# Optimization experiments

Hardware: AMD Instinct MI355X
Metric: run time of the kernel (lower is better)

The kernel has to match this reference:

```python
import jax, jax.numpy as jnp
import numpy as np

B, S, D = 2, 2048, 1024
E, N, HID = 8, 4, 4096

def setup_inputs() -> dict:
    key = jax.random.key(0)
    ks = jax.random.split(key, 6)
    x = jax.random.normal(ks[0], (B, S, D), dtype=jnp.float32)
    w_router = jax.random.normal(ks[1], (E, D), dtype=jnp.float32) * 0.02
    A_fc = jax.random.normal(ks[2], (E, N, N, N), dtype=jnp.float32) * 0.5
    S_fc = jax.random.normal(ks[3], (E, N, HID // N, D // N), dtype=jnp.float32) * (1.0 / np.sqrt(D))
    A_proj = jax.random.normal(ks[4], (E, N, N, N), dtype=jnp.float32) * 0.5
    S_proj = jax.random.normal(ks[5], (E, N, D // N, HID // N), dtype=jnp.float32) * (1.0 / np.sqrt(HID))
    return {"x": x, "w_router": w_router, "A_fc": A_fc, "S_fc": S_fc, "A_proj": A_proj, "S_proj": S_proj}

def _phm(Xn, A, S):
    # Xn: [T, n, s_in], S: [n, s_out, s_in], A: [n, n, n] -> [T, n, s_out]
    T_ = jnp.einsum('bkl,iol->bkio', Xn, S)
    return jnp.einsum('ijk,bkio->bjo', A, T_)

def reference(x, w_router, A_fc, S_fc, A_proj, S_proj):
    e_num, n = A_fc.shape[0], A_fc.shape[1]
    d = x.shape[-1]
    flat = x.reshape(-1, d)                      # [T, D]
    T = flat.shape[0]
    logits = flat @ w_router.T                   # [T, E]
    probs = jax.nn.softmax(logits, axis=-1)
    expert_idx = jnp.argmax(logits, axis=-1)     # [T]
    tpe = jnp.zeros((e_num,), flat.dtype).at[expert_idx].add(1.0)
    frac = tpe / T
    aux_loss = jnp.sum(frac * probs.mean(axis=0)) * e_num
    Xn = flat.reshape(T, n, d // n)
    out = jnp.zeros_like(flat)
    for e in range(e_num):                        # small fixed expert loop
        h = _phm(Xn, A_fc[e], S_fc[e]).reshape(T, -1)   # [T, HID]
        h = jnp.where(h >= 0, h, 0.5 * h)               # leaky_relu slope 0.5
        Hn = (h * h).reshape(T, n, -1)
        y = _phm(Hn, A_proj[e], S_proj[e]).reshape(T, d)
        out = out + jnp.where((expert_idx == e)[:, None], y, jnp.zeros((), flat.dtype))
    return out.reshape(x.shape), aux_loss
```

## Files before the change

### kernel.cpp

```cpp
#include <hip/hip_runtime.h>
#include <hip/hip_bf16.h>


#define T_TOK 4096
#define DIM   1024
#define NEXP  8
#define HIDD  4096
#define SLOTS 5120

static constexpr size_t OFF_WFC   = 0;
static constexpr size_t OFF_WPROJ = 67108864ull;
static constexpr size_t OFF_XB    = 134217728ull;
static constexpr size_t OFF_H     = 144703488ull;
static constexpr size_t OFF_PROBS = 186646528ull;
static constexpr size_t OFF_EIDX  = OFF_PROBS + (size_t)T_TOK*8*4;
static constexpr size_t OFF_TOK   = OFF_EIDX + (size_t)T_TOK*4;
static constexpr size_t OFF_CNT   = OFF_TOK + (size_t)SLOTS*4;

typedef __attribute__((ext_vector_type(8))) short short8;
typedef __attribute__((ext_vector_type(4))) float f32x4;

static __device__ __forceinline__ ushort f2bf(float f) {
    __hip_bfloat16 h = __float2bfloat16(f);
    return __builtin_bit_cast(ushort, h);
}

static __device__ __forceinline__ void gload_lds16(const ushort* g, ushort* l) {
    __builtin_amdgcn_global_load_lds((const __attribute__((address_space(1))) void*)g,
                                     (__attribute__((address_space(3))) void*)l,
                                     16, 0, 0);
}

__global__ __launch_bounds__(256) void router_k(const float* __restrict__ x,
                                                const float* __restrict__ wr,
                                                float* __restrict__ probs,
                                                int* __restrict__ eidx,
                                                ushort* __restrict__ xb)
{
    int tid = threadIdx.x, w = tid >> 6, lane = tid & 63;
    int t = blockIdx.x * 4 + w;
    const float4* xr = (const float4*)(x + (size_t)t * DIM);
    float4 xv[4];
#pragma unroll
    for (int q = 0; q < 4; q++) xv[q] = xr[q * 64 + lane];
    ushort4* xo = (ushort4*)(xb + (size_t)t * DIM);
#pragma unroll
    for (int q = 0; q < 4; q++) {
        float4 v = xv[q];
        ushort4 bq;
        bq.x = f2bf(v.x); bq.y = f2bf(v.y); bq.z = f2bf(v.z); bq.w = f2bf(v.w);
        xo[q * 64 + lane] = bq;
    }
    double lg[8];
#pragma unroll
    for (int e = 0; e < 8; e++) {
        const float4* wv = (const float4*)(wr + (size_t)e * DIM);
        double s = 0.0;
#pragma unroll
        for (int q = 0; q < 4; q++) {
            float4 a = xv[q], b = wv[q * 64 + lane];
            s += (double)a.x * b.x + (double)a.y * b.y + (double)a.z * b.z + (double)a.w * b.w;
        }
#pragma unroll
        for (int d = 1; d < 64; d <<= 1) s += __shfl_xor(s, d);
        lg[e] = s;
    }
    double m = lg[0];
#pragma unroll
    for (int e = 1; e < 8; e++) m = lg[e] > m ? lg[e] : m;
    double ex[8], sum = 0.0;
#pragma unroll
    for (int e = 0; e < 8; e++) { ex[e] = exp(lg[e] - m); sum += ex[e]; }
    if (lane < 8) probs[(size_t)t * 8 + lane] = (float)(ex[lane] / sum);
    if (lane == 0) {
        int am = 0; double bv = lg[0];
#pragma unroll
        for (int e = 1; e < 8; e++) if (lg[e] > bv) { bv = lg[e]; am = e; }
        eidx[t] = am;
    }
}

__global__ __launch_bounds__(256) void plan_k(const float* __restrict__ probs,
                                              const int* __restrict__ eidx,
                                              int* __restrict__ counts,
                                              int* __restrict__ offsets,
                                              int* __restrict__ tok,
                                              float* __restrict__ auxout)
{
    __shared__ int hist[256][8];
    __shared__ double red[256][8];
    __shared__ int offs[8];
    int tid = threadIdx.x;
    for (int i = tid; i < SLOTS; i += 256) tok[i] = -1;
    int base = tid * 16;
    int le[16];
    int lc[8] = {0,0,0,0,0,0,0,0};
#pragma unroll
    for (int j = 0; j < 16; j++) { le[j] = eidx[base + j]; lc[le[j]]++; }
#pragma unroll
    for (int e = 0; e < 8; e++) hist[tid][e] = lc[e];
    __syncthreads();
    for (int s = 1; s < 256; s <<= 1) {
        int v[8];
        if (tid >= s) {
#pragma unroll
            for (int e = 0; e < 8; e++) v[e] = hist[tid - s][e];
        }
        __syncthreads();
        if (tid >= s) {
#pragma unroll
            for (int e = 0; e < 8; e++) hist[tid][e] += v[e];
        }
        __syncthreads();
    }
    int myBase[8];
#pragma unroll
    for (int e = 0; e < 8; e++) myBase[e] = hist[tid][e] - lc[e];
    if (tid == 0) {
        int off = 0;
#pragma unroll
        for (int e = 0; e < 8; e++) {
            int c = hist[255][e];
            counts[e] = c;
            offsets[e] = off; offs[e] = off;
            off += (c + 127) & ~127;
        }
    }
    __syncthreads();
    int cur[8];
#pragma unroll
    for (int e = 0; e < 8; e++) cur[e] = myBase[e];
#pragma unroll
    for (int j = 0; j < 16; j++) {
        int e = le[j];
        tok[offs[e] + cur[e]++] = base + j;
    }
    double ps[8] = {0, 0, 0, 0, 0, 0, 0, 0};
    for (int t = tid; t < T_TOK; t += 256) {
#pragma unroll
        for (int e = 0; e < 8; e++) ps[e] += (double)probs[(size_t)t * 8 + e];
    }
#pragma unroll
    for (int e = 0; e < 8; e++) red[tid][e] = ps[e];
    __syncthreads();
    for (int s = 128; s > 0; s >>= 1) {
        if (tid < s) {
#pragma unroll
            for (int e = 0; e < 8; e++) red[tid][e] += red[tid + s][e];
        }
        __syncthreads();
    }
    if (tid == 0) {
        double aux = 0.0;
#pragma unroll
        for (int e = 0; e < 8; e++)
            aux += ((double)hist[255][e] / T_TOK) * (red[0][e] / T_TOK);
        auxout[0] = (float)(aux * NEXP);
    }
}

__global__ __launch_bounds__(256) void wfc_k(const float* __restrict__ A,
                                             const float* __restrict__ S,
                                             ushort* __restrict__ W)
{
    int b = blockIdx.x;
    int e = b >> 10, o = b & 1023;
    int l = threadIdx.x;
    __shared__ float Ash[64];
    if (l < 64) Ash[l] = A[e * 64 + l];
    __syncthreads();
    float s0 = S[((size_t)(e * 4 + 0) * 1024 + o) * 256 + l];
    float s1 = S[((size_t)(e * 4 + 1) * 1024 + o) * 256 + l];
    float s2 = S[((size_t)(e * 4 + 2) * 1024 + o) * 256 + l];
    float s3 = S[((size_t)(e * 4 + 3) * 1024 + o) * 256 + l];
    size_t base = (size_t)e * 4194304ull;
#pragma unroll
    for (int j = 0; j < 4; j++)
#pragma unroll
        for (int k = 0; k < 4; k++) {
            float v = Ash[j * 4 + k] * s0 + Ash[16 + j * 4 + k] * s1 +
                      Ash[32 + j * 4 + k] * s2 + Ash[48 + j * 4 + k] * s3;
            W[base + (size_t)(j * 1024 + o) * 1024 + k * 256 + l] = f2bf(v);
        }
}

__global__ __launch_bounds__(256) void wpj_k(const float* __restrict__ A,
                                             const float* __restrict__ S,
                                             ushort* __restrict__ W)
{
    int b = blockIdx.x;
    int e = b >> 8, o = b & 255;
    int tid = threadIdx.x;
    __shared__ float Ash[64];
    if (tid < 64) Ash[tid] = A[e * 64 + tid];
    __syncthreads();
    float s[4][4];
#pragma unroll
    for (int i = 0; i < 4; i++)
#pragma unroll
        for (int q = 0; q < 4; q++)
            s[i][q] = S[((size_t)(e * 4 + i) * 256 + o) * 1024 + q * 256 + tid];
    size_t base = (size_t)e * 4194304ull;
#pragma unroll
    for (int j = 0; j < 4; j++)
#pragma unroll
        for (int k = 0; k < 4; k++) {
            float a0 = Ash[j * 4 + k], a1 = Ash[16 + j * 4 + k];
            float a2 = Ash[32 + j * 4 + k], a3 = Ash[48 + j * 4 + k];
#pragma unroll
            for (int q = 0; q < 4; q++) {
                float v = a0 * s[0][q] + a1 * s[1][q] + a2 * s[2][q] + a3 * s[3][q];
                W[base + (size_t)(j * 256 + o) * 4096 + k * 1024 + q * 256 + tid] = f2bf(v);
            }
        }
}

template <int KDIM, int NDIM, int NSPLIT, bool FC>
__global__ __launch_bounds__(256, 2) void moe_gemm_k(const ushort* __restrict__ Abuf,
                                                     const ushort* __restrict__ Wbuf,
                                                     ushort* __restrict__ Hout,
                                                     float* __restrict__ Yout,
                                                     const int* __restrict__ counts,
                                                     const int* __restrict__ offsets,
                                                     const int* __restrict__ tok)
{
    __shared__ __align__(16) ushort As[128 * 64];
    __shared__ __align__(16) ushort Bs[256 * 64];
    constexpr int KSUB = KDIM / NSPLIT;
    constexpr int NT = KSUB / 64;
    int b = blockIdx.x;
    int nb, split, ms;
    if (FC) {
        int r = b >> 3;
        nb = (b & 7) * 2 + r / 40;
        split = 0;
        ms = r % 40;
    } else {
        nb = (b & 7) >> 1;
        split = b & 1;
        ms = b >> 3;
    }
    int e = -1, mt = 0, acct = 0;
#pragma unroll
    for (int i = 0; i < 8; i++) {
        int tiles = (counts[i] + 127) >> 7;
        if (e < 0 && ms < acct + tiles) { e = i; mt = ms - acct; }
        acct += tiles;
    }
    if (e < 0) return;
    int m_base = offsets[e] + mt * 128;
    int n_base = nb * 256;
    int tid = threadIdx.x, w = tid >> 6, lane = tid & 63;
    int wm = w >> 1, wn = w & 1;
    const ushort* Bb = Wbuf + (size_t)e * NDIM * KDIM + (size_t)n_base * KDIM;
    int lr = lane >> 3;
    int lcs = (((lane & 7) ^ lr) << 3);
    const ushort* arow[4];
#pragma unroll
    for (int i = 0; i < 4; i++) {
        int sl = m_base + i * 32 + w * 8 + lr;
        int rt = sl;
        if (FC) { rt = tok[sl]; if (rt < 0) rt = 0; }
        arow[i] = Abuf + (size_t)rt * KDIM + lcs;
    }
    f32x4 acc[4][8];
#pragma unroll
    for (int i = 0; i < 4; i++)
#pragma unroll
        for (int j = 0; j < 8; j++) acc[i][j] = (f32x4){0.f, 0.f, 0.f, 0.f};

    for (int t = 0; t < NT; t++) {
        int k0 = split * KSUB + t * 64;
#pragma unroll
        for (int i = 0; i < 4; i++)
            gload_lds16(arow[i] + k0, &As[(i * 32 + w * 8) * 64]);
#pragma unroll
        for (int i = 0; i < 8; i++) {
            int r0 = i * 32 + w * 8;
            gload_lds16(Bb + (size_t)(r0 + lr) * KDIM + k0 + lcs, &Bs[r0 * 64]);
        }
        __syncthreads();
#pragma unroll
        for (int ks = 0; ks < 2; ks++) {
            short8 a[4], bfr[8];
#pragma unroll
            for (int f = 0; f < 4; f++) {
                int ra = wm * 64 + f * 16 + (lane & 15);
                int ca = (((ks * 4 + (lane >> 4)) ^ (lane & 7)) << 3);
                a[f] = *(const short8*)&As[ra * 64 + ca];
            }
#pragma unroll
            for (int f = 0; f < 8; f++) {
                int rb = wn * 128 + f * 16 + (lane & 15);
                int ca = (((ks * 4 + (lane >> 4)) ^ (lane & 7)) << 3);
                bfr[f] = *(const short8*)&Bs[rb * 64 + ca];
            }
#pragma unroll
            for (int mf = 0; mf < 4; mf++)
#pragma unroll
                for (int nf = 0; nf < 8; nf++)
                    acc[mf][nf] = __builtin_amdgcn_mfma_f32_16x16x32_bf16(a[mf], bfr[nf], acc[mf][nf], 0, 0, 0);
        }
        __syncthreads();
    }

    int col0 = n_base + wn * 128;
    int row0 = wm * 64 + (lane >> 4) * 4;
    if (FC) {
#pragma unroll
        for (int mf = 0; mf < 4; mf++)
#pragma unroll
            for (int nf = 0; nf < 8; nf++) {
                int col = col0 + nf * 16 + (lane & 15);
#pragma unroll
                for (int rg = 0; rg < 4; rg++) {
                    float v = acc[mf][nf][rg];
                    v = v >= 0.f ? v : 0.5f * v;
                    v = v * v;
                    Hout[(size_t)(m_base + row0 + mf * 16 + rg) * NDIM + col] = f2bf(v);
                }
            }
    } else {
        float* P = Yout + (size_t)split * SLOTS * NDIM;
#pragma unroll
        for (int mf = 0; mf < 4; mf++)
#pragma unroll
            for (int nf = 0; nf < 8; nf++) {
                int col = col0 + nf * 16 + (lane & 15);
#pragma unroll
                for (int rg = 0; rg < 4; rg++)
                    P[(size_t)(m_base + row0 + mf * 16 + rg) * NDIM + col] = acc[mf][nf][rg];
            }
    }
}

__global__ __launch_bounds__(256) void reduce_k(const float* __restrict__ P,
                                                const int* __restrict__ tok,
                                                float* __restrict__ out)
{
    int slot = blockIdx.x;
    int t = tok[slot];
    if (t < 0) return;
    const float4* p0 = (const float4*)(P + (size_t)slot * DIM);
    const float4* p1 = (const float4*)(P + (size_t)(SLOTS + slot) * DIM);
    float4* o = (float4*)(out + (size_t)t * DIM);
    int i = threadIdx.x;
    float4 a = p0[i], b = p1[i];
    o[i] = (float4){a.x + b.x, a.y + b.y, a.z + b.z, a.w + b.w};
}

extern "C" void kernel_launch(void* const* d_in, const int* in_sizes, int n_in,
                              void* d_out, int out_size, void* d_ws, size_t ws_size,
                              hipStream_t stream)
{
    const float* x    = (const float*)d_in[0];
    const float* wr   = (const float*)d_in[1];
    const float* A_fc = (const float*)d_in[2];
    const float* S_fc = (const float*)d_in[3];
    const float* A_pj = (const float*)d_in[4];
    const float* S_pj = (const float*)d_in[5];
    float* out = (float*)d_out;
    char* ws = (char*)d_ws;

    ushort* Wfc   = (ushort*)(ws + OFF_WFC);
    float*  Part  = (float*)(ws + OFF_WFC);
    ushort* Wpj   = (ushort*)(ws + OFF_WPROJ);
    ushort* xb    = (ushort*)(ws + OFF_XB);
    ushort* h     = (ushort*)(ws + OFF_H);
    float*  probs = (float*)(ws + OFF_PROBS);
    int*    eidx  = (int*)(ws + OFF_EIDX);
    int*    tok   = (int*)(ws + OFF_TOK);
    int*    counts  = (int*)(ws + OFF_CNT);
    int*    offsets = counts + 16;

    router_k<<<T_TOK / 4, 256, 0, stream>>>(x, wr, probs, eidx, xb);
    plan_k<<<1, 256, 0, stream>>>(probs, eidx, counts, offsets, tok,
                                  out + (size_t)T_TOK * DIM);
    wfc_k<<<NEXP * 1024, 256, 0, stream>>>(A_fc, S_fc, Wfc);
    wpj_k<<<NEXP * 256, 256, 0, stream>>>(A_pj, S_pj, Wpj);
    moe_gemm_k<1024, 4096, 1, true><<<640, 256, 0, stream>>>(xb, Wfc, h, nullptr, counts, offsets, tok);
    moe_gemm_k<4096, 1024, 2, false><<<320, 256, 0, stream>>>(h, Wpj, nullptr, Part, counts, offsets, tok);
    reduce_k<<<SLOTS, 256, 0, stream>>>(Part, tok, out);
}
```

Baseline: 190.9 us.

## Triple-buffer MoE GEMM LDS tiles with 512-thread blocks and async prefetch

Restructures the expert GEMM kernel to use 8 waves per block (2x4 wave grid, 64x64 per wave) and a three-stage LDS ring buffer. The next-next K tile is prefetched with direct-to-LDS loads while the current one is computed, using explicit vmcnt waits and raw barriers in place of two __syncthreads per iteration. MFMA sections are wrapped in s_setprio. The aim is to hide global-load latency and raise occupancy, at the cost of triple the LDS footprint (144KB per block), which may limit resident blocks per CU.

Result: slower. 229.6 us (+20.3%).

```diff
diff --git a/kernel.cpp b/kernel.cpp
--- a/kernel.cpp
+++ b/kernel.cpp
@@ -216,7 +216,7 @@
 }
 
 template <int KDIM, int NDIM, int NSPLIT, bool FC>
-__global__ __launch_bounds__(256, 2) void moe_gemm_k(const ushort* __restrict__ Abuf,
+__global__ __launch_bounds__(512, 4) void moe_gemm_k(const ushort* __restrict__ Abuf,
                                                      const ushort* __restrict__ Wbuf,
                                                      ushort* __restrict__ Hout,
                                                      float* __restrict__ Yout,
@@ -224,8 +224,8 @@
                                                      const int* __restrict__ offsets,
                                                      const int* __restrict__ tok)
 {
-    __shared__ __align__(16) ushort As[128 * 64];
-    __shared__ __align__(16) ushort Bs[256 * 64];
+    __shared__ __align__(16) ushort As[3][128 * 64];
+    __shared__ __align__(16) ushort Bs[3][256 * 64];
     constexpr int KSUB = KDIM / NSPLIT;
     constexpr int NT = KSUB / 64;
     int b = blockIdx.x;
@@ -251,66 +251,78 @@
     int m_base = offsets[e] + mt * 128;
     int n_base = nb * 256;
     int tid = threadIdx.x, w = tid >> 6, lane = tid & 63;
-    int wm = w >> 1, wn = w & 1;
+    int wm = w >> 2, wn = w & 3;
     const ushort* Bb = Wbuf + (size_t)e * NDIM * KDIM + (size_t)n_base * KDIM;
     int lr = lane >> 3;
     int lcs = (((lane & 7) ^ lr) << 3);
-    const ushort* arow[4];
-#pragma unroll
-    for (int i = 0; i < 4; i++) {
-        int sl = m_base + i * 32 + w * 8 + lr;
+    int kbase = split * KSUB;
+    const ushort* arow[2];
+#pragma unroll
+    for (int i = 0; i < 2; i++) {
+        int sl = m_base + i * 64 + w * 8 + lr;
         int rt = sl;
         if (FC) { rt = tok[sl]; if (rt < 0) rt = 0; }
-        arow[i] = Abuf + (size_t)rt * KDIM + lcs;
-    }
-    f32x4 acc[4][8];
+        arow[i] = Abuf + (size_t)rt * KDIM + kbase + lcs;
+    }
+    const ushort* brow[4];
 #pragma unroll
     for (int i = 0; i < 4; i++)
-#pragma unroll
-        for (int j = 0; j < 8; j++) acc[i][j] = (f32x4){0.f, 0.f, 0.f, 0.f};
-
+        brow[i] = Bb + (size_t)(i * 64 + w * 8 + lr) * KDIM + kbase + lcs;
+
+    f32x4 acc[4][4];
+#pragma unroll
+    for (int i = 0; i < 4; i++)
+#pragma unroll
+        for (int j = 0; j < 4; j++) acc[i][j] = (f32x4){0.f, 0.f, 0.f, 0.f};
+
+    auto STAGE = [&](int kt, int q) {
+        int k0 = kt * 64;
+#pragma unroll
+        for (int i = 0; i < 2; i++)
+            gload_lds16(arow[i] + k0, &As[q][(i * 64 + w * 8) * 64]);
+#pragma unroll
+        for (int i = 0; i < 4; i++)
+            gload_lds16(brow[i] + k0, &Bs[q][(i * 64 + w * 8) * 64]);
+    };
+
+    STAGE(0, 0);
+    STAGE(1, 1);
+
+    int q = 0;
     for (int t = 0; t < NT; t++) {
-        int k0 = split * KSUB + t * 64;
-#pragma unroll
-        for (int i = 0; i < 4; i++)
-            gload_lds16(arow[i] + k0, &As[(i * 32 + w * 8) * 64]);
-#pragma unroll
-        for (int i = 0; i < 8; i++) {
-            int r0 = i * 32 + w * 8;
-            gload_lds16(Bb + (size_t)(r0 + lr) * KDIM + k0 + lcs, &Bs[r0 * 64]);
-        }
-        __syncthreads();
+        if (t == NT - 1) { asm volatile("s_waitcnt vmcnt(0)" ::: "memory"); }
+        else             { asm volatile("s_waitcnt vmcnt(6)" ::: "memory"); }
+        __builtin_amdgcn_s_barrier();
+        __builtin_amdgcn_sched_barrier(0);
+        if (t + 2 < NT) STAGE(t + 2, (q + 2) % 3);
 #pragma unroll
         for (int ks = 0; ks < 2; ks++) {
-            short8 a[4], bfr[8];
+            short8 a[4], bb[4];
+            int ca = (((ks * 4 + (lane >> 4)) ^ (lane & 7)) << 3);
 #pragma unroll
             for (int f = 0; f < 4; f++) {
-                int ra = wm * 64 + f * 16 + (lane & 15);
-                int ca = (((ks * 4 + (lane >> 4)) ^ (lane & 7)) << 3);
-                a[f] = *(const short8*)&As[ra * 64 + ca];
+                a[f]  = *(const short8*)&As[q][(wm * 64 + f * 16 + (lane & 15)) * 64 + ca];
+                bb[f] = *(const short8*)&Bs[q][(wn * 64 + f * 16 + (lane & 15)) * 64 + ca];
             }
-#pragma unroll
-            for (int f = 0; f < 8; f++) {
-                int rb = wn * 128 + f * 16 + (lane & 15);
-                int ca = (((ks * 4 + (lane >> 4)) ^ (lane & 7)) << 3);
-                bfr[f] = *(const short8*)&Bs[rb * 64 + ca];
-            }
+            __builtin_amdgcn_s_setprio(1);
 #pragma unroll
             for (int mf = 0; mf < 4; mf++)
 #pragma unroll
-                for (int nf = 0; nf < 8; nf++)
-                    acc[mf][nf] = __builtin_amdgcn_mfma_f32_16x16x32_bf16(a[mf], bfr[nf], acc[mf][nf], 0, 0, 0);
-        }
-        __syncthreads();
-    }
-
-    int col0 = n_base + wn * 128;
+                for (int nf = 0; nf < 4; nf++)
+                    acc[mf][nf] = __builtin_amdgcn_mfma_f32_16x16x32_bf16(a[mf], bb[nf], acc[mf][nf], 0, 0, 0);
+            __builtin_amdgcn_s_setprio(0);
+        }
+        __builtin_amdgcn_s_barrier();
+        q = (q + 1) % 3;
+    }
+
+    int col0 = n_base + wn * 64;
     int row0 = wm * 64 + (lane >> 4) * 4;
     if (FC) {
 #pragma unroll
         for (int mf = 0; mf < 4; mf++)
 #pragma unroll
-            for (int nf = 0; nf < 8; nf++) {
+            for (int nf = 0; nf < 4; nf++) {
                 int col = col0 + nf * 16 + (lane & 15);
 #pragma unroll
                 for (int rg = 0; rg < 4; rg++) {
@@ -325,7 +337,7 @@
 #pragma unroll
         for (int mf = 0; mf < 4; mf++)
 #pragma unroll
-            for (int nf = 0; nf < 8; nf++) {
+            for (int nf = 0; nf < 4; nf++) {
                 int col = col0 + nf * 16 + (lane & 15);
 #pragma unroll
                 for (int rg = 0; rg < 4; rg++)
@@ -378,7 +390,7 @@
                                   out + (size_t)T_TOK * DIM);
     wfc_k<<<NEXP * 1024, 256, 0, stream>>>(A_fc, S_fc, Wfc);
     wpj_k<<<NEXP * 256, 256, 0, stream>>>(A_pj, S_pj, Wpj);
-    moe_gemm_k<1024, 4096, 1, true><<<640, 256, 0, stream>>>(xb, Wfc, h, nullptr, counts, offsets, tok);
-    moe_gemm_k<4096, 1024, 2, false><<<320, 256, 0, stream>>>(h, Wpj, nullptr, Part, counts, offsets, tok);
+    moe_gemm_k<1024, 4096, 1, true><<<640, 512, 0, stream>>>(xb, Wfc, h, nullptr, counts, offsets, tok);
+    moe_gemm_k<4096, 1024, 2, false><<<320, 512, 0, stream>>>(h, Wpj, nullptr, Part, counts, offsets, tok);
     reduce_k<<<SLOTS, 256, 0, stream>>>(Part, tok, out);
 }
```

## Drop split-K and reduce pass, scatter proj output directly; merge weight kernels

Applied to the files above, without the earlier changes.

The projection GEMM no longer splits K in two with a separate reduce kernel. It now uses 64-row M tiles with four N-slices per block and scatters results straight to the output rows via the token map. The two weight-construction kernels are merged into one launch. The router emits per-block prob sums instead of per-token probs, so the planner reads less. This removes the partial-buffer write/read and two launches, at the cost of longer per-block K loops and a different tile shape for the proj GEMM.

Result: slower. 195.3 us (+2.3%).

```diff
diff --git a/kernel.cpp b/kernel.cpp
--- a/kernel.cpp
+++ b/kernel.cpp
@@ -12,8 +12,8 @@
 static constexpr size_t OFF_WPROJ = 67108864ull;
 static constexpr size_t OFF_XB    = 134217728ull;
 static constexpr size_t OFF_H     = 144703488ull;
-static constexpr size_t OFF_PROBS = 186646528ull;
-static constexpr size_t OFF_EIDX  = OFF_PROBS + (size_t)T_TOK*8*4;
+static constexpr size_t OFF_BSUM  = 186646528ull;
+static constexpr size_t OFF_EIDX  = OFF_BSUM + 1024*8*8;
 static constexpr size_t OFF_TOK   = OFF_EIDX + (size_t)T_TOK*4;
 static constexpr size_t OFF_CNT   = OFF_TOK + (size_t)SLOTS*4;
 
@@ -33,10 +33,11 @@
 
 __global__ __launch_bounds__(256) void router_k(const float* __restrict__ x,
                                                 const float* __restrict__ wr,
-                                                float* __restrict__ probs,
+                                                double* __restrict__ bsum,
                                                 int* __restrict__ eidx,
                                                 ushort* __restrict__ xb)
 {
+    __shared__ double shp[4][8];
     int tid = threadIdx.x, w = tid >> 6, lane = tid & 63;
     int t = blockIdx.x * 4 + w;
     const float4* xr = (const float4*)(x + (size_t)t * DIM);
@@ -71,16 +72,20 @@
     double ex[8], sum = 0.0;
 #pragma unroll
     for (int e = 0; e < 8; e++) { ex[e] = exp(lg[e] - m); sum += ex[e]; }
-    if (lane < 8) probs[(size_t)t * 8 + lane] = (float)(ex[lane] / sum);
+    if (lane < 8) shp[w][lane] = ex[lane] / sum;
     if (lane == 0) {
         int am = 0; double bv = lg[0];
 #pragma unroll
         for (int e = 1; e < 8; e++) if (lg[e] > bv) { bv = lg[e]; am = e; }
         eidx[t] = am;
     }
-}
-
-__global__ __launch_bounds__(256) void plan_k(const float* __restrict__ probs,
+    __syncthreads();
+    if (tid < 8)
+        bsum[(size_t)blockIdx.x * 8 + tid] =
+            shp[0][tid] + shp[1][tid] + shp[2][tid] + shp[3][tid];
+}
+
+__global__ __launch_bounds__(256) void plan_k(const double* __restrict__ bsum,
                                               const int* __restrict__ eidx,
                                               int* __restrict__ counts,
                                               int* __restrict__ offsets,
@@ -136,9 +141,9 @@
         tok[offs[e] + cur[e]++] = base + j;
     }
     double ps[8] = {0, 0, 0, 0, 0, 0, 0, 0};
-    for (int t = tid; t < T_TOK; t += 256) {
-#pragma unroll
-        for (int e = 0; e < 8; e++) ps[e] += (double)probs[(size_t)t * 8 + e];
+    for (int b = tid; b < 1024; b += 256) {
+#pragma unroll
+        for (int e = 0; e < 8; e++) ps[e] += bsum[(size_t)b * 8 + e];
     }
 #pragma unroll
     for (int e = 0; e < 8; e++) red[tid][e] = ps[e];
@@ -159,63 +164,61 @@
     }
 }
 
-__global__ __launch_bounds__(256) void wfc_k(const float* __restrict__ A,
-                                             const float* __restrict__ S,
-                                             ushort* __restrict__ W)
-{
+__global__ __launch_bounds__(256) void wmat_k(const float* __restrict__ Afc,
+                                              const float* __restrict__ Sfc,
+                                              const float* __restrict__ Apj,
+                                              const float* __restrict__ Spj,
+                                              ushort* __restrict__ Wfc,
+                                              ushort* __restrict__ Wpj)
+{
+    __shared__ float Ash[64];
     int b = blockIdx.x;
-    int e = b >> 10, o = b & 1023;
-    int l = threadIdx.x;
-    __shared__ float Ash[64];
-    if (l < 64) Ash[l] = A[e * 64 + l];
-    __syncthreads();
-    float s0 = S[((size_t)(e * 4 + 0) * 1024 + o) * 256 + l];
-    float s1 = S[((size_t)(e * 4 + 1) * 1024 + o) * 256 + l];
-    float s2 = S[((size_t)(e * 4 + 2) * 1024 + o) * 256 + l];
-    float s3 = S[((size_t)(e * 4 + 3) * 1024 + o) * 256 + l];
-    size_t base = (size_t)e * 4194304ull;
-#pragma unroll
-    for (int j = 0; j < 4; j++)
-#pragma unroll
-        for (int k = 0; k < 4; k++) {
-            float v = Ash[j * 4 + k] * s0 + Ash[16 + j * 4 + k] * s1 +
-                      Ash[32 + j * 4 + k] * s2 + Ash[48 + j * 4 + k] * s3;
-            W[base + (size_t)(j * 1024 + o) * 1024 + k * 256 + l] = f2bf(v);
-        }
-}
-
-__global__ __launch_bounds__(256) void wpj_k(const float* __restrict__ A,
-                                             const float* __restrict__ S,
-                                             ushort* __restrict__ W)
-{
-    int b = blockIdx.x;
-    int e = b >> 8, o = b & 255;
     int tid = threadIdx.x;
-    __shared__ float Ash[64];
-    if (tid < 64) Ash[tid] = A[e * 64 + tid];
-    __syncthreads();
-    float s[4][4];
-#pragma unroll
-    for (int i = 0; i < 4; i++)
-#pragma unroll
-        for (int q = 0; q < 4; q++)
-            s[i][q] = S[((size_t)(e * 4 + i) * 256 + o) * 1024 + q * 256 + tid];
-    size_t base = (size_t)e * 4194304ull;
-#pragma unroll
-    for (int j = 0; j < 4; j++)
-#pragma unroll
-        for (int k = 0; k < 4; k++) {
-            float a0 = Ash[j * 4 + k], a1 = Ash[16 + j * 4 + k];
-            float a2 = Ash[32 + j * 4 + k], a3 = Ash[48 + j * 4 + k];
-#pragma unroll
-            for (int q = 0; q < 4; q++) {
-                float v = a0 * s[0][q] + a1 * s[1][q] + a2 * s[2][q] + a3 * s[3][q];
-                W[base + (size_t)(j * 256 + o) * 4096 + k * 1024 + q * 256 + tid] = f2bf(v);
-            }
-        }
-}
-
-template <int KDIM, int NDIM, int NSPLIT, bool FC>
+    if (b < 8192) {
+        int e = b >> 10, o = b & 1023;
+        if (tid < 64) Ash[tid] = Afc[e * 64 + tid];
+        __syncthreads();
+        float s0 = Sfc[((size_t)(e * 4 + 0) * 1024 + o) * 256 + tid];
+        float s1 = Sfc[((size_t)(e * 4 + 1) * 1024 + o) * 256 + tid];
+        float s2 = Sfc[((size_t)(e * 4 + 2) * 1024 + o) * 256 + tid];
+        float s3 = Sfc[((size_t)(e * 4 + 3) * 1024 + o) * 256 + tid];
+        size_t base = (size_t)e * 4194304ull;
+#pragma unroll
+        for (int j = 0; j < 4; j++)
+#pragma unroll
+            for (int k = 0; k < 4; k++) {
+                float v = Ash[j * 4 + k] * s0 + Ash[16 + j * 4 + k] * s1 +
+                          Ash[32 + j * 4 + k] * s2 + Ash[48 + j * 4 + k] * s3;
+                Wfc[base + (size_t)(j * 1024 + o) * 1024 + k * 256 + tid] = f2bf(v);
+            }
+    } else {
+        int b2 = b - 8192;
+        int e = b2 >> 8, o = b2 & 255;
+        if (tid < 64) Ash[tid] = Apj[e * 64 + tid];
+        __syncthreads();
+        float s[4][4];
+#pragma unroll
+        for (int i = 0; i < 4; i++)
+#pragma unroll
+            for (int q = 0; q < 4; q++)
+                s[i][q] = Spj[((size_t)(e * 4 + i) * 256 + o) * 1024 + q * 256 + tid];
+        size_t base = (size_t)e * 4194304ull;
+#pragma unroll
+        for (int j = 0; j < 4; j++)
+#pragma unroll
+            for (int k = 0; k < 4; k++) {
+                float a0 = Ash[j * 4 + k], a1 = Ash[16 + j * 4 + k];
+                float a2 = Ash[32 + j * 4 + k], a3 = Ash[48 + j * 4 + k];
+#pragma unroll
+                for (int q = 0; q < 4; q++) {
+                    float v = a0 * s[0][q] + a1 * s[1][q] + a2 * s[2][q] + a3 * s[3][q];
+                    Wpj[base + (size_t)(j * 256 + o) * 4096 + k * 1024 + q * 256 + tid] = f2bf(v);
+                }
+            }
+    }
+}
+
+template <int KDIM, int NDIM, int BM, bool FC>
 __global__ __launch_bounds__(256, 2) void moe_gemm_k(const ushort* __restrict__ Abuf,
                                                      const ushort* __restrict__ Wbuf,
                                                      ushort* __restrict__ Hout,
@@ -224,55 +227,55 @@
                                                      const int* __restrict__ offsets,
                                                      const int* __restrict__ tok)
 {
-    __shared__ __align__(16) ushort As[128 * 64];
+    __shared__ __align__(16) ushort As[BM * 64];
     __shared__ __align__(16) ushort Bs[256 * 64];
-    constexpr int KSUB = KDIM / NSPLIT;
-    constexpr int NT = KSUB / 64;
+    constexpr int NT = KDIM / 64;
+    constexpr int NF = FC ? 8 : 4;
+    constexpr int WNC = FC ? 128 : 64;
     int b = blockIdx.x;
-    int nb, split, ms;
+    int nb, ms;
     if (FC) {
         int r = b >> 3;
         nb = (b & 7) * 2 + r / 40;
-        split = 0;
         ms = r % 40;
     } else {
-        nb = (b & 7) >> 1;
-        split = b & 1;
-        ms = b >> 3;
+        nb = b & 3;
+        ms = b >> 2;
     }
     int e = -1, mt = 0, acct = 0;
 #pragma unroll
     for (int i = 0; i < 8; i++) {
-        int tiles = (counts[i] + 127) >> 7;
+        int tiles = (counts[i] + BM - 1) / BM;
         if (e < 0 && ms < acct + tiles) { e = i; mt = ms - acct; }
         acct += tiles;
     }
     if (e < 0) return;
-    int m_base = offsets[e] + mt * 128;
+    int m_base = offsets[e] + mt * BM;
     int n_base = nb * 256;
     int tid = threadIdx.x, w = tid >> 6, lane = tid & 63;
-    int wm = w >> 1, wn = w & 1;
+    int wm = FC ? (w >> 1) : 0;
+    int wn = FC ? (w & 1) : w;
     const ushort* Bb = Wbuf + (size_t)e * NDIM * KDIM + (size_t)n_base * KDIM;
     int lr = lane >> 3;
     int lcs = (((lane & 7) ^ lr) << 3);
-    const ushort* arow[4];
-#pragma unroll
-    for (int i = 0; i < 4; i++) {
+    const ushort* arow[BM / 32];
+#pragma unroll
+    for (int i = 0; i < BM / 32; i++) {
         int sl = m_base + i * 32 + w * 8 + lr;
         int rt = sl;
         if (FC) { rt = tok[sl]; if (rt < 0) rt = 0; }
         arow[i] = Abuf + (size_t)rt * KDIM + lcs;
     }
-    f32x4 acc[4][8];
+    f32x4 acc[4][NF];
 #pragma unroll
     for (int i = 0; i < 4; i++)
 #pragma unroll
-        for (int j = 0; j < 8; j++) acc[i][j] = (f32x4){0.f, 0.f, 0.f, 0.f};
+        for (int j = 0; j < NF; j++) acc[i][j] = (f32x4){0.f, 0.f, 0.f, 0.f};
 
     for (int t = 0; t < NT; t++) {
-        int k0 = split * KSUB + t * 64;
-#pragma unroll
-        for (int i = 0; i < 4; i++)
+        int k0 = t * 64;
+#pragma unroll
+        for (int i = 0; i < BM / 32; i++)
             gload_lds16(arow[i] + k0, &As[(i * 32 + w * 8) * 64]);
 #pragma unroll
         for (int i = 0; i < 8; i++) {
@@ -282,35 +285,30 @@
         __syncthreads();
 #pragma unroll
         for (int ks = 0; ks < 2; ks++) {
-            short8 a[4], bfr[8];
-#pragma unroll
-            for (int f = 0; f < 4; f++) {
-                int ra = wm * 64 + f * 16 + (lane & 15);
-                int ca = (((ks * 4 + (lane >> 4)) ^ (lane & 7)) << 3);
-                a[f] = *(const short8*)&As[ra * 64 + ca];
-            }
-#pragma unroll
-            for (int f = 0; f < 8; f++) {
-                int rb = wn * 128 + f * 16 + (lane & 15);
-                int ca = (((ks * 4 + (lane >> 4)) ^ (lane & 7)) << 3);
-                bfr[f] = *(const short8*)&Bs[rb * 64 + ca];
-            }
+            short8 a[4], bfr[NF];
+            int ca = (((ks * 4 + (lane >> 4)) ^ (lane & 7)) << 3);
+#pragma unroll
+            for (int f = 0; f < 4; f++)
+                a[f] = *(const short8*)&As[(wm * 64 + f * 16 + (lane & 15)) * 64 + ca];
+#pragma unroll
+            for (int f = 0; f < NF; f++)
+                bfr[f] = *(const short8*)&Bs[(wn * WNC + f * 16 + (lane & 15)) * 64 + ca];
 #pragma unroll
             for (int mf = 0; mf < 4; mf++)
 #pragma unroll
-                for (int nf = 0; nf < 8; nf++)
+                for (int nf = 0; nf < NF; nf++)
                     acc[mf][nf] = __builtin_amdgcn_mfma_f32_16x16x32_bf16(a[mf], bfr[nf], acc[mf][nf], 0, 0, 0);
         }
         __syncthreads();
     }
 
-    int col0 = n_base + wn * 128;
+    int col0 = n_base + wn * WNC;
     int row0 = wm * 64 + (lane >> 4) * 4;
     if (FC) {
 #pragma unroll
         for (int mf = 0; mf < 4; mf++)
 #pragma unroll
-            for (int nf = 0; nf < 8; nf++) {
+            for (int nf = 0; nf < NF; nf++) {
                 int col = col0 + nf * 16 + (lane & 15);
 #pragma unroll
                 for (int rg = 0; rg < 4; rg++) {
@@ -321,32 +319,25 @@
                 }
             }
     } else {
-        float* P = Yout + (size_t)split * SLOTS * NDIM;
-#pragma unroll
-        for (int mf = 0; mf < 4; mf++)
-#pragma unroll
-            for (int nf = 0; nf < 8; nf++) {
+        int limit = offsets[e] + counts[e];
+#pragma unroll
+        for (int mf = 0; mf < 4; mf++) {
+            int tk[4]; bool vld[4];
+#pragma unroll
+            for (int rg = 0; rg < 4; rg++) {
+                int slot = m_base + row0 + mf * 16 + rg;
+                vld[rg] = slot < limit;
+                tk[rg] = vld[rg] ? tok[slot] : 0;
+            }
+#pragma unroll
+            for (int nf = 0; nf < NF; nf++) {
                 int col = col0 + nf * 16 + (lane & 15);
 #pragma unroll
                 for (int rg = 0; rg < 4; rg++)
-                    P[(size_t)(m_base + row0 + mf * 16 + rg) * NDIM + col] = acc[mf][nf][rg];
-            }
-    }
-}
-
-__global__ __launch_bounds__(256) void reduce_k(const float* __restrict__ P,
-                                                const int* __restrict__ tok,
-                                                float* __restrict__ out)
-{
-    int slot = blockIdx.x;
-    int t = tok[slot];
-    if (t < 0) return;
-    const float4* p0 = (const float4*)(P + (size_t)slot * DIM);
-    const float4* p1 = (const float4*)(P + (size_t)(SLOTS + slot) * DIM);
-    float4* o = (float4*)(out + (size_t)t * DIM);
-    int i = threadIdx.x;
-    float4 a = p0[i], b = p1[i];
-    o[i] = (float4){a.x + b.x, a.y + b.y, a.z + b.z, a.w + b.w};
+                    if (vld[rg]) Yout[(size_t)tk[rg] * NDIM + col] = acc[mf][nf][rg];
+            }
+        }
+    }
 }
 
 extern "C" void kernel_launch(void* const* d_in, const int* in_sizes, int n_in,
@@ -363,22 +354,19 @@
     char* ws = (char*)d_ws;
 
     ushort* Wfc   = (ushort*)(ws + OFF_WFC);
-    float*  Part  = (float*)(ws + OFF_WFC);
     ushort* Wpj   = (ushort*)(ws + OFF_WPROJ);
     ushort* xb    = (ushort*)(ws + OFF_XB);
     ushort* h     = (ushort*)(ws + OFF_H);
-    float*  probs = (float*)(ws + OFF_PROBS);
+    double* bsum  = (double*)(ws + OFF_BSUM);
     int*    eidx  = (int*)(ws + OFF_EIDX);
     int*    tok   = (int*)(ws + OFF_TOK);
     int*    counts  = (int*)(ws + OFF_CNT);
     int*    offsets = counts + 16;
 
-    router_k<<<T_TOK / 4, 256, 0, stream>>>(x, wr, probs, eidx, xb);
-    plan_k<<<1, 256, 0, stream>>>(probs, eidx, counts, offsets, tok,
+    router_k<<<T_TOK / 4, 256, 0, stream>>>(x, wr, bsum, eidx, xb);
+    plan_k<<<1, 256, 0, stream>>>(bsum, eidx, counts, offsets, tok,
                                   out + (size_t)T_TOK * DIM);
-    wfc_k<<<NEXP * 1024, 256, 0, stream>>>(A_fc, S_fc, Wfc);
-    wpj_k<<<NEXP * 256, 256, 0, stream>>>(A_pj, S_pj, Wpj);
-    moe_gemm_k<1024, 4096, 1, true><<<640, 256, 0, stream>>>(xb, Wfc, h, nullptr, counts, offsets, tok);
-    moe_gemm_k<4096, 1024, 2, false><<<320, 256, 0, stream>>>(h, Wpj, nullptr, Part, counts, offsets, tok);
-    reduce_k<<<SLOTS, 256, 0, stream>>>(Part, tok, out);
-}
+    wmat_k<<<10240, 256, 0, stream>>>(A_fc, S_fc, A_pj, S_pj, Wfc, Wpj);
+    moe_gemm_k<1024, 4096, 128, true><<<640, 256, 0, stream>>>(xb, Wfc, h, nullptr, counts, offsets, tok);
+    moe_gemm_k<4096, 1024, 64, false><<<320, 256, 0, stream>>>(h, Wpj, nullptr, out, counts, offsets, tok);
+}
```
